# Kernel tuning notes

Measured on AMD Instinct MI355X. Metric: run time of the kernel, lower is better.

Reference implementation:

```python
import jax, jax.numpy as jnp
import numpy as np

N, NFEAT, NHID, K = 10000, 3000, 32, 10
ALPHA = 0.2


def setup_inputs() -> dict:
    key = jax.random.key(0)
    k1, k2, k3, k4, k5 = jax.random.split(key, 5)
    stdv = 1.0 / np.sqrt(NHID)
    x = jax.random.normal(k1, (N, NFEAT), dtype=jnp.float32)
    adj = jax.random.uniform(k2, (N, N), dtype=jnp.float32) / N  # row-stochastic-ish
    W = jax.random.uniform(k3, (NFEAT, NHID), minval=-stdv, maxval=stdv, dtype=jnp.float32)
    b = jax.random.uniform(k4, (NHID,), minval=-stdv, maxval=stdv, dtype=jnp.float32)
    mu = jax.random.normal(k5, (K, NHID), dtype=jnp.float32)
    return {"x": x, "adj": adj, "W": W, "b": b, "mu": mu}


def reference(x, adj, W, b, mu):
    # GCN layer: adj @ (x @ W) + b
    support = jnp.matmul(x, W)            # [N, NHID]
    z = jnp.matmul(adj, support) + b      # [N, NHID]
    # Student-t soft assignment (computed without materializing [N, K, NHID]):
    # ||z_i - mu_j||^2 = |z_i|^2 - 2 z_i.mu_j + |mu_j|^2
    z2 = jnp.sum(z * z, axis=1, keepdims=True)        # [N, 1]
    mu2 = jnp.sum(mu * mu, axis=1)                    # [K]
    d2 = z2 - 2.0 * jnp.matmul(z, mu.T) + mu2         # [N, K]
    q = 1.0 / (1.0 + d2 / ALPHA + 1e-08)
    q = q ** (ALPHA + 1.0) / 2.0
    q = q / jnp.sum(q, axis=1, keepdims=True)
    return z, q
```

## Files before the change

kernel.cpp:

```cpp
#include <hip/hip_runtime.h>
#include <math.h>


#define NH     32
#define KC     32
#define TR     256
#define LDA_S  36
#define NSPLIT 16

__global__ __launch_bounds__(256) void gemm_nt32(
    const float* __restrict__ A,
    const float* __restrict__ B,
    float* __restrict__ outp,
    int M, int K, int nchunks)
{
    __shared__ float As[TR * LDA_S];
    __shared__ float Bs[KC * NH];

    const int tid  = threadIdx.x;
    const int rg   = tid >> 2;
    const int jg   = tid & 3;
    const int row0 = blockIdx.x * TR;
    const int sy   = blockIdx.y;

    float acc[4][8];
#pragma unroll
    for (int m = 0; m < 4; ++m)
#pragma unroll
        for (int j = 0; j < 8; ++j) acc[m][j] = 0.0f;

    for (int c = sy; c < nchunks; c += NSPLIT) {
        const int k0 = c * KC;

#pragma unroll
        for (int p = 0; p < 8; ++p) {
            int idx = tid + (p << 8);
            int ar  = idx >> 3;
            int ac4 = idx & 7;
            int gr  = row0 + ar;
            int gk  = k0 + (ac4 << 2);
            float4 v = make_float4(0.f, 0.f, 0.f, 0.f);
            if (gr < M && gk < K)
                v = *(const float4*)(A + (size_t)gr * K + gk);
            *(float4*)(&As[ar * LDA_S + (ac4 << 2)]) = v;
        }
        {
            int brow = tid >> 3;
            int bc4  = tid & 7;
            int gk   = k0 + brow;
            float4 v = make_float4(0.f, 0.f, 0.f, 0.f);
            if (gk < K)
                v = *(const float4*)(B + (size_t)gk * NH + (bc4 << 2));
            *(float4*)(&Bs[brow * NH + (bc4 << 2)]) = v;
        }
        __syncthreads();

#pragma unroll
        for (int kk = 0; kk < KC; kk += 4) {
            float4 a[4];
#pragma unroll
            for (int m = 0; m < 4; ++m)
                a[m] = *(const float4*)(&As[(rg + (m << 6)) * LDA_S + kk]);
#pragma unroll
            for (int t = 0; t < 4; ++t) {
                float4 b0 = *(const float4*)(&Bs[(kk + t) * NH + (jg << 3)]);
                float4 b1 = *(const float4*)(&Bs[(kk + t) * NH + (jg << 3) + 4]);
#pragma unroll
                for (int m = 0; m < 4; ++m) {
                    float av = (t == 0) ? a[m].x : (t == 1) ? a[m].y
                             : (t == 2) ? a[m].z : a[m].w;
                    acc[m][0] += av * b0.x;
                    acc[m][1] += av * b0.y;
                    acc[m][2] += av * b0.z;
                    acc[m][3] += av * b0.w;
                    acc[m][4] += av * b1.x;
                    acc[m][5] += av * b1.y;
                    acc[m][6] += av * b1.z;
                    acc[m][7] += av * b1.w;
                }
            }
        }
        __syncthreads();
    }

    float* op = outp + (size_t)sy * M * NH;
#pragma unroll
    for (int m = 0; m < 4; ++m) {
        int gr = row0 + rg + (m << 6);
        if (gr < M) {
            float4 v0 = make_float4(acc[m][0], acc[m][1], acc[m][2], acc[m][3]);
            float4 v1 = make_float4(acc[m][4], acc[m][5], acc[m][6], acc[m][7]);
            *(float4*)(op + (size_t)gr * NH + (jg << 3))     = v0;
            *(float4*)(op + (size_t)gr * NH + (jg << 3) + 4) = v1;
        }
    }
}

__global__ __launch_bounds__(256) void reduce_add(
    const float* __restrict__ parts,
    const float* __restrict__ bias,
    float* __restrict__ out,
    int total4)
{
    int i = blockIdx.x * blockDim.x + threadIdx.x;
    if (i >= total4) return;
    float4 s = make_float4(0.f, 0.f, 0.f, 0.f);
#pragma unroll
    for (int p = 0; p < NSPLIT; ++p) {
        float4 v = ((const float4*)parts)[(size_t)p * total4 + i];
        s.x += v.x; s.y += v.y; s.z += v.z; s.w += v.w;
    }
    if (bias) {
        float4 bv = ((const float4*)bias)[i & 7];
        s.x += bv.x; s.y += bv.y; s.z += bv.z; s.w += bv.w;
    }
    ((float4*)out)[i] = s;
}

__global__ __launch_bounds__(256) void qkern(
    const float* __restrict__ z,
    const float* __restrict__ mu,
    float* __restrict__ q,
    int N)
{
    const int tid  = threadIdx.x;
    const int lane = tid & 31;
    const int i    = blockIdx.x * 8 + (tid >> 5);
    if (i >= N) return;

    float zv = z[i * 32 + lane];
    float qm = 0.f, qsum = 0.f;
#pragma unroll
    for (int c = 0; c < 10; ++c) {
        float d = zv - mu[c * 32 + lane];
        float p = d * d;
#pragma unroll
        for (int m = 16; m >= 1; m >>= 1) p += __shfl_xor(p, m, 32);
        float t  = 1.0f + p * 5.0f + 1e-8f;
        float qc = powf(t, -1.2f) * 0.5f;
        qsum += qc;
        if (lane == c) qm = qc;
    }
    if (lane < 10) q[i * 10 + lane] = qm / qsum;
}

extern "C" void kernel_launch(void* const* d_in, const int* in_sizes, int n_in,
                              void* d_out, int out_size, void* d_ws, size_t ws_size,
                              hipStream_t stream)
{
    const float* x   = (const float*)d_in[0];
    const float* adj = (const float*)d_in[1];
    const float* W   = (const float*)d_in[2];
    const float* b   = (const float*)d_in[3];
    const float* mu  = (const float*)d_in[4];

    const int N = 10000, NFEAT = 3000;
    float* z_out = (float*)d_out;
    float* q_out = (float*)d_out + N * NH;

    float* ws_part    = (float*)d_ws;
    float* ws_support = (float*)d_ws + (size_t)NSPLIT * N * NH;

    const int total4   = N * NH / 4;
    const int rowBlks  = (N + TR - 1) / TR;
    const int redBlks  = (total4 + 255) / 256;

    {
        int nchunks = (NFEAT + KC - 1) / KC;
        gemm_nt32<<<dim3(rowBlks, NSPLIT), 256, 0, stream>>>(
            x, W, ws_part, N, NFEAT, nchunks);
    }
    reduce_add<<<redBlks, 256, 0, stream>>>(ws_part, nullptr, ws_support, total4);
    {
        int nchunks = (N + KC - 1) / KC;
        gemm_nt32<<<dim3(rowBlks, NSPLIT), 256, 0, stream>>>(
            adj, ws_support, ws_part, N, N, nchunks);
    }
    reduce_add<<<redBlks, 256, 0, stream>>>(ws_part, b, z_out, total4);
    qkern<<<(N + 7) / 8, 256, 0, stream>>>(z_out, mu, q_out, N);
}
```

Before: 835.4 us.

## Double-buffer GEMM tiles with register prefetch and shrink row tile

Reworks the skinny GEMM kernel to prefetch the next K-chunk into registers while computing on the current shared-memory buffer, using two LDS buffers so only one barrier per iteration is needed. Row tile drops from 256 to 128 rows, with each thread owning 4 rows by 4 columns, and the split-K factor changes from 16 to 13. A launch-bounds occupancy hint of 3 is added. The aim is to hide global-load latency in this bandwidth-bound adj pass, at the cost of more register pressure and a different grid shape.

```diff
diff --git a/kernel.cpp b/kernel.cpp
--- a/kernel.cpp
+++ b/kernel.cpp
@@ -4,95 +4,129 @@
 
 #define NH     32
 #define KC     32
-#define TR     256
-#define LDA_S  36
-#define NSPLIT 16
-
-__global__ __launch_bounds__(256) void gemm_nt32(
+#define TR     128
+#define PAD_S  34
+#define NSPLIT 13
+
+__global__ __launch_bounds__(256, 3) void gemm_v2(
     const float* __restrict__ A,
     const float* __restrict__ B,
     float* __restrict__ outp,
     int M, int K, int nchunks)
 {
-    __shared__ float As[TR * LDA_S];
-    __shared__ float Bs[KC * NH];
+    __shared__ float As[2][TR * PAD_S];
+    __shared__ float Bs[2][KC * NH];
 
     const int tid  = threadIdx.x;
-    const int rg   = tid >> 2;
-    const int jg   = tid & 3;
+    const int rg   = tid >> 3;
+    const int jg   = tid & 7;
     const int row0 = blockIdx.x * TR;
     const int sy   = blockIdx.y;
 
-    float acc[4][8];
-#pragma unroll
-    for (int m = 0; m < 4; ++m)
-#pragma unroll
-        for (int j = 0; j < 8; ++j) acc[m][j] = 0.0f;
-
+    const int b_kl = tid >> 3;
+    const int b_c4 = tid & 7;
+
+    float4 acc[4];
+#pragma unroll
+    for (int m = 0; m < 4; ++m) acc[m] = make_float4(0.f, 0.f, 0.f, 0.f);
+
+    float4 Ar[4];
+    float4 Br;
+
+    {
+        const int k0 = sy * KC;
+#pragma unroll
+        for (int p = 0; p < 4; ++p) {
+            int a  = p * 256 + tid;
+            int rl = a >> 3, c4 = a & 7;
+            int gr = row0 + rl;
+            int gk = k0 + (c4 << 2);
+            Ar[p] = make_float4(0.f, 0.f, 0.f, 0.f);
+            if (gr < M && gk < K)
+                Ar[p] = *(const float4*)(A + (size_t)gr * K + gk);
+        }
+        {
+            int gk = k0 + b_kl;
+            Br = make_float4(0.f, 0.f, 0.f, 0.f);
+            if (gk < K)
+                Br = *(const float4*)(B + (size_t)gk * NH + (b_c4 << 2));
+        }
+#pragma unroll
+        for (int p = 0; p < 4; ++p) {
+            int a  = p * 256 + tid;
+            int rl = a >> 3, c4 = a & 7;
+            *(float4*)(&As[0][rl * PAD_S + (c4 << 2)]) = Ar[p];
+        }
+        *(float4*)(&Bs[0][b_kl * NH + (b_c4 << 2)]) = Br;
+    }
+
+    int buf = 0;
     for (int c = sy; c < nchunks; c += NSPLIT) {
-        const int k0 = c * KC;
-
-#pragma unroll
-        for (int p = 0; p < 8; ++p) {
-            int idx = tid + (p << 8);
-            int ar  = idx >> 3;
-            int ac4 = idx & 7;
-            int gr  = row0 + ar;
-            int gk  = k0 + (ac4 << 2);
-            float4 v = make_float4(0.f, 0.f, 0.f, 0.f);
-            if (gr < M && gk < K)
-                v = *(const float4*)(A + (size_t)gr * K + gk);
-            *(float4*)(&As[ar * LDA_S + (ac4 << 2)]) = v;
-        }
-        {
-            int brow = tid >> 3;
-            int bc4  = tid & 7;
-            int gk   = k0 + brow;
-            float4 v = make_float4(0.f, 0.f, 0.f, 0.f);
+        __syncthreads();
+
+        const int cn = c + NSPLIT;
+        const bool has_next = (cn < nchunks);
+
+        if (has_next) {
+            const int k0 = cn * KC;
+#pragma unroll
+            for (int p = 0; p < 4; ++p) {
+                int a  = p * 256 + tid;
+                int rl = a >> 3, c4 = a & 7;
+                int gr = row0 + rl;
+                int gk = k0 + (c4 << 2);
+                Ar[p] = make_float4(0.f, 0.f, 0.f, 0.f);
+                if (gr < M && gk < K)
+                    Ar[p] = *(const float4*)(A + (size_t)gr * K + gk);
+            }
+            int gk = cn * KC + b_kl;
+            Br = make_float4(0.f, 0.f, 0.f, 0.f);
             if (gk < K)
-                v = *(const float4*)(B + (size_t)gk * NH + (bc4 << 2));
-            *(float4*)(&Bs[brow * NH + (bc4 << 2)]) = v;
-        }
-        __syncthreads();
-
-#pragma unroll
-        for (int kk = 0; kk < KC; kk += 4) {
+                Br = *(const float4*)(B + (size_t)gk * NH + (b_c4 << 2));
+        }
+
+        const float* Ab = &As[buf][0];
+        const float* Bb = &Bs[buf][0];
+#pragma unroll
+        for (int kq = 0; kq < 8; ++kq) {
             float4 a[4];
 #pragma unroll
             for (int m = 0; m < 4; ++m)
-                a[m] = *(const float4*)(&As[(rg + (m << 6)) * LDA_S + kk]);
+                a[m] = *(const float4*)(Ab + (rg + (m << 5)) * PAD_S + (kq << 2));
 #pragma unroll
             for (int t = 0; t < 4; ++t) {
-                float4 b0 = *(const float4*)(&Bs[(kk + t) * NH + (jg << 3)]);
-                float4 b1 = *(const float4*)(&Bs[(kk + t) * NH + (jg << 3) + 4]);
+                float4 b = *(const float4*)(Bb + ((kq << 2) + t) * NH + (jg << 2));
 #pragma unroll
                 for (int m = 0; m < 4; ++m) {
                     float av = (t == 0) ? a[m].x : (t == 1) ? a[m].y
                              : (t == 2) ? a[m].z : a[m].w;
-                    acc[m][0] += av * b0.x;
-                    acc[m][1] += av * b0.y;
-                    acc[m][2] += av * b0.z;
-                    acc[m][3] += av * b0.w;
-                    acc[m][4] += av * b1.x;
-                    acc[m][5] += av * b1.y;
-                    acc[m][6] += av * b1.z;
-                    acc[m][7] += av * b1.w;
+                    acc[m].x += av * b.x;
+                    acc[m].y += av * b.y;
+                    acc[m].z += av * b.z;
+                    acc[m].w += av * b.w;
                 }
             }
         }
-        __syncthreads();
+
+        if (has_next) {
+            const int nb = buf ^ 1;
+#pragma unroll
+            for (int p = 0; p < 4; ++p) {
+                int a  = p * 256 + tid;
+                int rl = a >> 3, c4 = a & 7;
+                *(float4*)(&As[nb][rl * PAD_S + (c4 << 2)]) = Ar[p];
+            }
+            *(float4*)(&Bs[nb][b_kl * NH + (b_c4 << 2)]) = Br;
+        }
+        buf ^= 1;
     }
 
     float* op = outp + (size_t)sy * M * NH;
 #pragma unroll
     for (int m = 0; m < 4; ++m) {
-        int gr = row0 + rg + (m << 6);
-        if (gr < M) {
-            float4 v0 = make_float4(acc[m][0], acc[m][1], acc[m][2], acc[m][3]);
-            float4 v1 = make_float4(acc[m][4], acc[m][5], acc[m][6], acc[m][7]);
-            *(float4*)(op + (size_t)gr * NH + (jg << 3))     = v0;
-            *(float4*)(op + (size_t)gr * NH + (jg << 3) + 4) = v1;
-        }
+        int gr = row0 + rg + (m << 5);
+        if (gr < M)
+            *(float4*)(op + (size_t)gr * NH + (jg << 2)) = acc[m];
     }
 }
 
@@ -161,19 +195,19 @@
     float* ws_part    = (float*)d_ws;
     float* ws_support = (float*)d_ws + (size_t)NSPLIT * N * NH;
 
-    const int total4   = N * NH / 4;
-    const int rowBlks  = (N + TR - 1) / TR;
-    const int redBlks  = (total4 + 255) / 256;
+    const int total4  = N * NH / 4;
+    const int rowBlks = (N + TR - 1) / TR;
+    const int redBlks = (total4 + 255) / 256;
 
     {
         int nchunks = (NFEAT + KC - 1) / KC;
-        gemm_nt32<<<dim3(rowBlks, NSPLIT), 256, 0, stream>>>(
+        gemm_v2<<<dim3(rowBlks, NSPLIT), 256, 0, stream>>>(
             x, W, ws_part, N, NFEAT, nchunks);
     }
     reduce_add<<<redBlks, 256, 0, stream>>>(ws_part, nullptr, ws_support, total4);
     {
         int nchunks = (N + KC - 1) / KC;
-        gemm_nt32<<<dim3(rowBlks, NSPLIT), 256, 0, stream>>>(
+        gemm_v2<<<dim3(rowBlks, NSPLIT), 256, 0, stream>>>(
             adj, ws_support, ws_part, N, N, nchunks);
     }
     reduce_add<<<redBlks, 256, 0, stream>>>(ws_part, b, z_out, total4);
```

Measured after the change: 1.149 ms. 1.38x slower.
